# Kernel tuning notes

Measured on AMD Instinct MI355X. Metric: run time of the kernel, lower is better.

## Reference

```python
import jax, jax.numpy as jnp
import numpy as np

DIM = 1024
N_HEADS = 16
HEAD_DIM = DIM // N_HEADS
SCALE = HEAD_DIM ** (-0.5)


def setup_inputs() -> dict:
    key = jax.random.key(0)
    ks = jax.random.split(key, 5)
    B, N = 2, 1024
    x = jax.random.normal(ks[0], (B, N, DIM), dtype=jnp.float32)
    # torch nn.Linear convention: weight is (out_features, in_features)
    w_qkvg = jax.random.normal(ks[1], (4 * DIM, DIM), dtype=jnp.float32) * (DIM ** -0.5)
    b_qkvg = jax.random.normal(ks[2], (4 * DIM,), dtype=jnp.float32) * 0.02
    w_proj = jax.random.normal(ks[3], (DIM, DIM), dtype=jnp.float32) * (DIM ** -0.5)
    b_proj = jax.random.normal(ks[4], (DIM,), dtype=jnp.float32) * 0.02
    return {"x": x, "w_qkvg": w_qkvg, "b_qkvg": b_qkvg, "w_proj": w_proj, "b_proj": b_proj}


def reference(x, w_qkvg, b_qkvg, w_proj, b_proj):
    B, N, dim = x.shape
    # fused qkvg projection: (B, N, 4*dim)
    qkvg = x @ w_qkvg.T + b_qkvg
    # (B, N, 4, H, hd) -> (4, B, H, N, hd)
    qkvg = qkvg.reshape(B, N, 4, N_HEADS, HEAD_DIM).transpose(2, 0, 3, 1, 4)
    q = jax.nn.softplus(qkvg[0])          # (B, H, N, hd)
    k = jax.nn.softplus(qkvg[1])          # (B, H, N, hd)
    v = jax.nn.gelu(qkvg[2], approximate=False)  # (B, H, N, hd)
    g = jax.nn.gelu(qkvg[3], approximate=False)  # (B, H, N, hd)
    # kv = k @ v^T over head_dim -> (B, H, N, N)
    kv = jnp.einsum('bhnd,bhmd->bhnm', k, v)
    # z: contract q over tokens with per-token k-sums -> (B, H, hd)
    z = jnp.einsum('bhcn,bhc->bhn', q, k.sum(axis=-1)) * SCALE
    z = 1.0 / (z + dim)
    # out[b,h,d,n] = sum_c q[b,h,c,n] * kv[b,h,c,d] -> (B, H, N, hd)
    out = jnp.einsum('bhcn,bhcd->bhdn', q, kv) * SCALE
    out = (out + v) * z[:, :, None, :]    # broadcast z over token axis
    out = out.reshape(B, N, dim)          # raw reshape, faithful to original
    out = out * g.reshape(B, N, dim)
    out = out @ w_proj.T + b_proj
    return out
```

## Files before the change

### kernel.cpp

```cpp
#include <hip/hip_runtime.h>
#include <hip/hip_bf16.h>
#include <math.h>

typedef float f32x4 __attribute__((ext_vector_type(4)));
typedef __bf16 bf16_t;
typedef bf16_t bf16x8 __attribute__((ext_vector_type(8)));
typedef bf16_t bf16x4 __attribute__((ext_vector_type(4)));

__device__ __forceinline__ void gload_lds16(const bf16_t* g, bf16_t* l) {
    __builtin_amdgcn_global_load_lds(
        (const __attribute__((address_space(1))) unsigned int*)g,
        (__attribute__((address_space(3))) unsigned int*)l, 16, 0, 0);
}

template<int N_IMM>
__device__ __forceinline__ void wait_vmcnt() {
    if constexpr (N_IMM == 0) asm volatile("s_waitcnt vmcnt(0)" ::: "memory");
    else if constexpr (N_IMM == 2) asm volatile("s_waitcnt vmcnt(2)" ::: "memory");
    else if constexpr (N_IMM == 3) asm volatile("s_waitcnt vmcnt(3)" ::: "memory");
    else if constexpr (N_IMM == 4) asm volatile("s_waitcnt vmcnt(4)" ::: "memory");
    else static_assert(N_IMM == 0, "unsupported vmcnt");
}

__global__ __launch_bounds__(256) void cvt3(const float* __restrict__ a, bf16_t* __restrict__ ao, int na4,
                                            const float* __restrict__ b, bf16_t* __restrict__ bo, int nb4,
                                            const float* __restrict__ c, bf16_t* __restrict__ co, int nc4) {
    int q = blockIdx.x * 256 + threadIdx.x;
    const float* src; bf16_t* dst;
    if (q < na4)            { src = a + (size_t)q * 4;              dst = ao + (size_t)q * 4; }
    else if (q < na4 + nb4) { int r = q - na4; src = b + (size_t)r * 4; dst = bo + (size_t)r * 4; }
    else if (q < na4 + nb4 + nc4) { int r = q - na4 - nb4; src = c + (size_t)r * 4; dst = co + (size_t)r * 4; }
    else return;
    float4 v = *reinterpret_cast<const float4*>(src);
    bf16x4 o;
    o[0] = (bf16_t)v.x; o[1] = (bf16_t)v.y; o[2] = (bf16_t)v.z; o[3] = (bf16_t)v.w;
    *reinterpret_cast<bf16x4*>(dst) = o;
}

template<int BM, int BN, int MR, int NR, int EPI>
__global__ __launch_bounds__(256) void gemm_bt(const bf16_t* __restrict__ A,
                                               const bf16_t* __restrict__ B,
                                               const float* __restrict__ bias,
                                               void* __restrict__ Cout,
                                               int M, int N) {
    constexpr int K = 1024;
    constexpr int TNUM = K / 32;
    constexpr int WCOLS = BN / (NR * 16);
    constexpr int WROWS = BM / (MR * 16);
    static_assert(WROWS * WCOLS == 4, "4 waves");
    constexpr int ASEG = BM / 64, BSEG = BN / 64;
    constexpr int LOADS = ASEG + BSEG;

    __shared__ __align__(16) bf16_t Sa0[BM * 32];
    __shared__ __align__(16) bf16_t Sb0[BN * 32];
    __shared__ __align__(16) bf16_t Sa1[BM * 32];
    __shared__ __align__(16) bf16_t Sb1[BN * 32];
    __shared__ __align__(16) bf16_t Sa2[BM * 32];
    __shared__ __align__(16) bf16_t Sb2[BN * 32];

    const int tid = threadIdx.x;
    const int lane = tid & 63;
    const int w = tid >> 6;
    const int wr = w / WCOLS, wc = w % WCOLS;

    const int NTM = M / BM, NTN = N / BN;
    const int CHM = NTM >> 3;
    const int chunkN = (NTN * CHM) >> 3;
    const int c = blockIdx.x & 7;
    const int pp = blockIdx.x >> 3;
    const int mt = (c % CHM) * 8 + (pp & 7);
    const int nt = (c / CHM) * chunkN + (pp >> 3);
    const int m0 = mt * BM, n0 = nt * BN;

    const int l15 = lane & 15, lg = lane >> 4;
    const int srow = lane >> 2, pos = lane & 3;

    f32x4 acc[MR][NR] = {};

    auto stageTo = [&](bf16_t* Ad, bf16_t* Bd, int k0) {
#pragma unroll
        for (int t = 0; t < ASEG; ++t) {
            int s = w + t * 4;
            int row = s * 16 + srow;
            int ch = pos ^ ((row >> 1) & 3);
            gload_lds16(&A[(size_t)(m0 + row) * K + k0 + ch * 8], &Ad[s * 512]);
        }
#pragma unroll
        for (int t = 0; t < BSEG; ++t) {
            int s = w + t * 4;
            int row = s * 16 + srow;
            int ch = pos ^ ((row >> 1) & 3);
            gload_lds16(&B[(size_t)(n0 + row) * K + k0 + ch * 8], &Bd[s * 512]);
        }
    };

    auto compute = [&](const bf16_t* Ac, const bf16_t* Bc) {
        bf16x8 af[MR], bfr[NR];
#pragma unroll
        for (int i = 0; i < MR; ++i) {
            int ar = wr * MR * 16 + i * 16 + l15;
            af[i] = *(const bf16x8*)(&Ac[ar * 32 + (lg ^ ((ar >> 1) & 3)) * 8]);
        }
#pragma unroll
        for (int j = 0; j < NR; ++j) {
            int br = wc * NR * 16 + j * 16 + l15;
            bfr[j] = *(const bf16x8*)(&Bc[br * 32 + (lg ^ ((br >> 1) & 3)) * 8]);
        }
#pragma unroll
        for (int i = 0; i < MR; ++i)
#pragma unroll
            for (int j = 0; j < NR; ++j)
                acc[i][j] = __builtin_amdgcn_mfma_f32_16x16x32_bf16(af[i], bfr[j], acc[i][j], 0, 0, 0);
    };

    stageTo(Sa0, Sb0, 0);
    stageTo(Sa1, Sb1, 32);

    for (int t = 0; t < TNUM - 2; t += 3) {
        wait_vmcnt<LOADS>();
        __builtin_amdgcn_s_barrier();
        __builtin_amdgcn_sched_barrier(0);
        stageTo(Sa2, Sb2, (t + 2) * 32);
        compute(Sa0, Sb0);
        __builtin_amdgcn_sched_barrier(0);

        wait_vmcnt<LOADS>();
        __builtin_amdgcn_s_barrier();
        __builtin_amdgcn_sched_barrier(0);
        stageTo(Sa0, Sb0, (t + 3) * 32);
        compute(Sa1, Sb1);
        __builtin_amdgcn_sched_barrier(0);

        wait_vmcnt<LOADS>();
        __builtin_amdgcn_s_barrier();
        __builtin_amdgcn_sched_barrier(0);
        stageTo(Sa1, Sb1, (t + 4) * 32);
        compute(Sa2, Sb2);
        __builtin_amdgcn_sched_barrier(0);
    }
    wait_vmcnt<LOADS>();
    __builtin_amdgcn_s_barrier();
    __builtin_amdgcn_sched_barrier(0);
    compute(Sa0, Sb0);
    __builtin_amdgcn_sched_barrier(0);

    wait_vmcnt<0>();
    __builtin_amdgcn_s_barrier();
    __builtin_amdgcn_sched_barrier(0);
    compute(Sa1, Sb1);

#pragma unroll
    for (int i = 0; i < MR; ++i) {
        int gm_base = m0 + wr * MR * 16 + i * 16 + lg * 4;
#pragma unroll
        for (int j = 0; j < NR; ++j) {
            int gn = n0 + wc * NR * 16 + j * 16 + l15;
            float bv = bias[gn];
#pragma unroll
            for (int r = 0; r < 4; ++r) {
                int gm = gm_base + r;
                float v = acc[i][j][r] + bv;
                if (EPI == 0) {
                    float a;
                    if ((gn >> 10) < 2) {
                        a = fmaxf(v, 0.f) + log1pf(expf(-fabsf(v)));
                    } else {
                        a = 0.5f * v * (1.f + erff(v * 0.70710678118654752f));
                    }
                    ((bf16_t*)Cout)[(size_t)gm * N + gn] = (bf16_t)a;
                } else {
                    ((float*)Cout)[(size_t)gm * N + gn] = v;
                }
            }
        }
    }
}

__global__ __launch_bounds__(256) void attn_A(const bf16_t* __restrict__ qkvg,
                                              float* __restrict__ Apart) {
    const int bh = blockIdx.x;
    const int p = blockIdx.y;
    const int b = bh >> 4, h = bh & 15;
    const int tid = threadIdx.x;
    __shared__ float ks[32][64];
    __shared__ float qs[32][64];
    float acc[4][4] = {};
    const int dg = tid >> 4, eg = tid & 15;
    const int stok = tid >> 3, se0 = (tid & 7) * 8;
    const size_t base = ((size_t)b * 1024) * 4096 + (size_t)h * 64;

    for (int t0 = p * 128; t0 < p * 128 + 128; t0 += 32) {
        __syncthreads();
        size_t rowb = base + (size_t)(t0 + stok) * 4096;
        bf16x8 qv8 = *(const bf16x8*)(&qkvg[rowb + se0]);
        bf16x8 kv8 = *(const bf16x8*)(&qkvg[rowb + 1024 + se0]);
#pragma unroll
        for (int jj = 0; jj < 8; ++jj) {
            qs[stok][se0 + jj] = (float)qv8[jj];
            ks[stok][se0 + jj] = (float)kv8[jj];
        }
        __syncthreads();
#pragma unroll 8
        for (int tt = 0; tt < 32; ++tt) {
            f32x4 kv = *(const f32x4*)(&ks[tt][dg * 4]);
            f32x4 qv = *(const f32x4*)(&qs[tt][eg * 4]);
#pragma unroll
            for (int i = 0; i < 4; ++i)
#pragma unroll
                for (int j = 0; j < 4; ++j) acc[i][j] += kv[i] * qv[j];
        }
    }
    float* dst = Apart + ((size_t)p * 32 + bh) * 4096;
#pragma unroll
    for (int i = 0; i < 4; ++i)
#pragma unroll
        for (int j = 0; j < 4; ++j)
            dst[(dg * 4 + i) * 64 + eg * 4 + j] = acc[i][j];
}

__global__ __launch_bounds__(256) void reduce_A_z(const float* __restrict__ Apart,
                                                  float* __restrict__ A,
                                                  float* __restrict__ z) {
    const int bh = blockIdx.x;
    const int tid = threadIdx.x;
    __shared__ float As[4096];
    for (int i0 = tid * 4; i0 < 4096; i0 += 1024) {
        f32x4 s = {};
#pragma unroll
        for (int p = 0; p < 8; ++p) {
            f32x4 v = *(const f32x4*)(&Apart[((size_t)p * 32 + bh) * 4096 + i0]);
            s += v;
        }
        *(f32x4*)(&As[i0]) = s;
        *(f32x4*)(&A[(size_t)bh * 4096 + i0]) = s;
    }
    __syncthreads();
    if (tid < 64) {
        float s = 0.f;
#pragma unroll 8
        for (int d = 0; d < 64; ++d) s += As[d * 64 + tid];
        z[bh * 64 + tid] = 1.0f / (s * 0.125f + 1024.0f);
    }
}

__global__ __launch_bounds__(256) void out_Y(const bf16_t* __restrict__ qkvg,
                                             const float* __restrict__ A,
                                             const float* __restrict__ z,
                                             bf16_t* __restrict__ Y) {
    const int bh = blockIdx.x;
    const int b = bh >> 4, h = bh & 15;
    const int chunk = blockIdx.y;
    const int tid = threadIdx.x;
    __shared__ float As[64][64];
    __shared__ float vs[32][64];
    __shared__ float zs[64];
    for (int i = tid; i < 4096; i += 256) As[i >> 6][i & 63] = A[(size_t)bh * 4096 + i];
    if (tid < 64) zs[tid] = z[bh * 64 + tid];
    const size_t base = ((size_t)b * 1024) * 4096 + (size_t)h * 64;
    const int e = tid & 63, trow = tid >> 6;
    const int stok = tid >> 3, se0 = (tid & 7) * 8;

    for (int t0 = chunk * 64; t0 < chunk * 64 + 64; t0 += 32) {
        __syncthreads();
        bf16x8 vv8 = *(const bf16x8*)(&qkvg[base + (size_t)(t0 + stok) * 4096 + 2048 + se0]);
#pragma unroll
        for (int jj = 0; jj < 8; ++jj) vs[stok][se0 + jj] = (float)vv8[jj];
        __syncthreads();
#pragma unroll
        for (int kk = 0; kk < 8; ++kk) {
            int ml = trow * 8 + kk;
            int m = t0 + ml;
            float s = 0.f;
#pragma unroll 8
            for (int d = 0; d < 64; ++d) s += vs[ml][d] * As[d][e];
            float g = (float)qkvg[base + (size_t)m * 4096 + 3072 + e];
            float o = (s * 0.125f + vs[ml][e]) * zs[e] * g;
            Y[((size_t)b * 1024 + h * 64 + (m >> 4)) * 1024 + ((m & 15) << 6) + e] = (bf16_t)o;
        }
    }
}

extern "C" void kernel_launch(void* const* d_in, const int* in_sizes, int n_in,
                              void* d_out, int out_size, void* d_ws, size_t ws_size,
                              hipStream_t stream) {
    const float* x      = (const float*)d_in[0];
    const float* w_qkvg = (const float*)d_in[1];
    const float* b_qkvg = (const float*)d_in[2];
    const float* w_proj = (const float*)d_in[3];
    const float* b_proj = (const float*)d_in[4];

    char* p = (char*)d_ws;
    bf16_t* xb    = (bf16_t*)p; p += (size_t)2048 * 1024 * 2;
    bf16_t* w1b   = (bf16_t*)p; p += (size_t)4096 * 1024 * 2;
    bf16_t* w2b   = (bf16_t*)p; p += (size_t)1024 * 1024 * 2;
    bf16_t* qkvg  = (bf16_t*)p; p += (size_t)2048 * 4096 * 2;
    float*  Apart = (float*)p;  p += (size_t)8 * 32 * 4096 * 4;
    float*  Afull = (float*)p;  p += (size_t)32 * 4096 * 4;
    float*  zbuf  = (float*)p;  p += (size_t)32 * 64 * 4;
    bf16_t* Ybuf  = (bf16_t*)p; p += (size_t)2048 * 1024 * 2;

    cvt3<<<7168, 256, 0, stream>>>(x, xb, 524288, w_qkvg, w1b, 1048576, w_proj, w2b, 262144);

    gemm_bt<128, 64, 4, 2, 0><<<1024, 256, 0, stream>>>(xb, w1b, b_qkvg, (void*)qkvg, 2048, 4096);
    attn_A<<<dim3(32, 8), 256, 0, stream>>>(qkvg, Apart);
    reduce_A_z<<<32, 256, 0, stream>>>(Apart, Afull, zbuf);
    out_Y<<<dim3(32, 16), 256, 0, stream>>>(qkvg, Afull, zbuf, Ybuf);
    gemm_bt<64, 64, 2, 2, 1><<<512, 256, 0, stream>>>(Ybuf, w2b, b_proj, d_out, 2048, 1024);
}
```

Before: 106.3 us.

## Move activations from QKVG GEMM epilogue into attention kernels with fp32 planar buffer

The fused QKVG projection is split into four separate GEMM launches, each writing a planar fp32 slab for q, k, v and g. Softplus and GELU are no longer applied in the GEMM epilogue; they are computed when the attention kernels load the data. This removes the divergent transcendental epilogue from the GEMM. In exchange, the intermediate buffer doubles in size, the GEMM uses smaller tiles and more launches, and activations are computed inside the attention kernels.

After: 114.4 us. 1.08x slower.

```diff
diff --git a/kernel.cpp b/kernel.cpp
--- a/kernel.cpp
+++ b/kernel.cpp
@@ -6,6 +6,13 @@
 typedef __bf16 bf16_t;
 typedef bf16_t bf16x8 __attribute__((ext_vector_type(8)));
 typedef bf16_t bf16x4 __attribute__((ext_vector_type(4)));
+
+__device__ __forceinline__ float act_softplus(float x) {
+    return fmaxf(x, 0.f) + log1pf(expf(-fabsf(x)));
+}
+__device__ __forceinline__ float act_gelu(float x) {
+    return 0.5f * x * (1.f + erff(x * 0.70710678118654752f));
+}
 
 __device__ __forceinline__ void gload_lds16(const bf16_t* g, bf16_t* l) {
     __builtin_amdgcn_global_load_lds(
@@ -37,11 +44,11 @@
     *reinterpret_cast<bf16x4*>(dst) = o;
 }
 
-template<int BM, int BN, int MR, int NR, int EPI>
+template<int BM, int BN, int MR, int NR>
 __global__ __launch_bounds__(256) void gemm_bt(const bf16_t* __restrict__ A,
                                                const bf16_t* __restrict__ B,
                                                const float* __restrict__ bias,
-                                               void* __restrict__ Cout,
+                                               float* __restrict__ Cout,
                                                int M, int N) {
     constexpr int K = 1024;
     constexpr int TNUM = K / 32;
@@ -159,24 +166,13 @@
 #pragma unroll
             for (int r = 0; r < 4; ++r) {
                 int gm = gm_base + r;
-                float v = acc[i][j][r] + bv;
-                if (EPI == 0) {
-                    float a;
-                    if ((gn >> 10) < 2) {
-                        a = fmaxf(v, 0.f) + log1pf(expf(-fabsf(v)));
-                    } else {
-                        a = 0.5f * v * (1.f + erff(v * 0.70710678118654752f));
-                    }
-                    ((bf16_t*)Cout)[(size_t)gm * N + gn] = (bf16_t)a;
-                } else {
-                    ((float*)Cout)[(size_t)gm * N + gn] = v;
-                }
+                Cout[(size_t)gm * N + gn] = acc[i][j][r] + bv;
             }
         }
     }
 }
 
-__global__ __launch_bounds__(256) void attn_A(const bf16_t* __restrict__ qkvg,
+__global__ __launch_bounds__(256) void attn_A(const float* __restrict__ qkvgf,
                                               float* __restrict__ Apart) {
     const int bh = blockIdx.x;
     const int p = blockIdx.y;
@@ -187,18 +183,24 @@
     float acc[4][4] = {};
     const int dg = tid >> 4, eg = tid & 15;
     const int stok = tid >> 3, se0 = (tid & 7) * 8;
-    const size_t base = ((size_t)b * 1024) * 4096 + (size_t)h * 64;
+    const float* qf = qkvgf;
+    const float* kf = qkvgf + (size_t)2048 * 1024;
 
     for (int t0 = p * 128; t0 < p * 128 + 128; t0 += 32) {
         __syncthreads();
-        size_t rowb = base + (size_t)(t0 + stok) * 4096;
-        bf16x8 qv8 = *(const bf16x8*)(&qkvg[rowb + se0]);
-        bf16x8 kv8 = *(const bf16x8*)(&qkvg[rowb + 1024 + se0]);
-#pragma unroll
-        for (int jj = 0; jj < 8; ++jj) {
-            qs[stok][se0 + jj] = (float)qv8[jj];
-            ks[stok][se0 + jj] = (float)kv8[jj];
-        }
+        size_t rowb = (size_t)(b * 1024 + t0 + stok) * 1024 + h * 64 + se0;
+        float4 q0 = *(const float4*)(&qf[rowb]);
+        float4 q1 = *(const float4*)(&qf[rowb + 4]);
+        float4 k0 = *(const float4*)(&kf[rowb]);
+        float4 k1 = *(const float4*)(&kf[rowb + 4]);
+        qs[stok][se0 + 0] = act_softplus(q0.x); qs[stok][se0 + 1] = act_softplus(q0.y);
+        qs[stok][se0 + 2] = act_softplus(q0.z); qs[stok][se0 + 3] = act_softplus(q0.w);
+        qs[stok][se0 + 4] = act_softplus(q1.x); qs[stok][se0 + 5] = act_softplus(q1.y);
+        qs[stok][se0 + 6] = act_softplus(q1.z); qs[stok][se0 + 7] = act_softplus(q1.w);
+        ks[stok][se0 + 0] = act_softplus(k0.x); ks[stok][se0 + 1] = act_softplus(k0.y);
+        ks[stok][se0 + 2] = act_softplus(k0.z); ks[stok][se0 + 3] = act_softplus(k0.w);
+        ks[stok][se0 + 4] = act_softplus(k1.x); ks[stok][se0 + 5] = act_softplus(k1.y);
+        ks[stok][se0 + 6] = act_softplus(k1.z); ks[stok][se0 + 7] = act_softplus(k1.w);
         __syncthreads();
 #pragma unroll 8
         for (int tt = 0; tt < 32; ++tt) {
@@ -243,7 +245,7 @@
     }
 }
 
-__global__ __launch_bounds__(256) void out_Y(const bf16_t* __restrict__ qkvg,
+__global__ __launch_bounds__(256) void out_Y(const float* __restrict__ qkvgf,
                                              const float* __restrict__ A,
                                              const float* __restrict__ z,
                                              bf16_t* __restrict__ Y) {
@@ -256,15 +258,20 @@
     __shared__ float zs[64];
     for (int i = tid; i < 4096; i += 256) As[i >> 6][i & 63] = A[(size_t)bh * 4096 + i];
     if (tid < 64) zs[tid] = z[bh * 64 + tid];
-    const size_t base = ((size_t)b * 1024) * 4096 + (size_t)h * 64;
+    const float* vf = qkvgf + (size_t)2 * 2048 * 1024;
+    const float* gf = qkvgf + (size_t)3 * 2048 * 1024;
     const int e = tid & 63, trow = tid >> 6;
     const int stok = tid >> 3, se0 = (tid & 7) * 8;
 
     for (int t0 = chunk * 64; t0 < chunk * 64 + 64; t0 += 32) {
         __syncthreads();
-        bf16x8 vv8 = *(const bf16x8*)(&qkvg[base + (size_t)(t0 + stok) * 4096 + 2048 + se0]);
-#pragma unroll
-        for (int jj = 0; jj < 8; ++jj) vs[stok][se0 + jj] = (float)vv8[jj];
+        size_t rowb = (size_t)(b * 1024 + t0 + stok) * 1024 + h * 64 + se0;
+        float4 v0 = *(const float4*)(&vf[rowb]);
+        float4 v1 = *(const float4*)(&vf[rowb + 4]);
+        vs[stok][se0 + 0] = act_gelu(v0.x); vs[stok][se0 + 1] = act_gelu(v0.y);
+        vs[stok][se0 + 2] = act_gelu(v0.z); vs[stok][se0 + 3] = act_gelu(v0.w);
+        vs[stok][se0 + 4] = act_gelu(v1.x); vs[stok][se0 + 5] = act_gelu(v1.y);
+        vs[stok][se0 + 6] = act_gelu(v1.z); vs[stok][se0 + 7] = act_gelu(v1.w);
         __syncthreads();
 #pragma unroll
         for (int kk = 0; kk < 8; ++kk) {
@@ -273,7 +280,7 @@
             float s = 0.f;
 #pragma unroll 8
             for (int d = 0; d < 64; ++d) s += vs[ml][d] * As[d][e];
-            float g = (float)qkvg[base + (size_t)m * 4096 + 3072 + e];
+            float g = act_gelu(gf[(size_t)(b * 1024 + m) * 1024 + h * 64 + e]);
             float o = (s * 0.125f + vs[ml][e]) * zs[e] * g;
             Y[((size_t)b * 1024 + h * 64 + (m >> 4)) * 1024 + ((m & 15) << 6) + e] = (bf16_t)o;
         }
@@ -293,7 +300,7 @@
     bf16_t* xb    = (bf16_t*)p; p += (size_t)2048 * 1024 * 2;
     bf16_t* w1b   = (bf16_t*)p; p += (size_t)4096 * 1024 * 2;
     bf16_t* w2b   = (bf16_t*)p; p += (size_t)1024 * 1024 * 2;
-    bf16_t* qkvg  = (bf16_t*)p; p += (size_t)2048 * 4096 * 2;
+    float*  qkvgf = (float*)p;  p += (size_t)4 * 2048 * 1024 * 4;
     float*  Apart = (float*)p;  p += (size_t)8 * 32 * 4096 * 4;
     float*  Afull = (float*)p;  p += (size_t)32 * 4096 * 4;
     float*  zbuf  = (float*)p;  p += (size_t)32 * 64 * 4;
@@ -301,9 +308,14 @@
 
     cvt3<<<7168, 256, 0, stream>>>(x, xb, 524288, w_qkvg, w1b, 1048576, w_proj, w2b, 262144);
 
-    gemm_bt<128, 64, 4, 2, 0><<<1024, 256, 0, stream>>>(xb, w1b, b_qkvg, (void*)qkvg, 2048, 4096);
-    attn_A<<<dim3(32, 8), 256, 0, stream>>>(qkvg, Apart);
+    for (int s = 0; s < 4; ++s) {
+        gemm_bt<64, 64, 2, 2><<<512, 256, 0, stream>>>(
+            xb, w1b + (size_t)s * 1024 * 1024, b_qkvg + s * 1024,
+            qkvgf + (size_t)s * 2048 * 1024, 2048, 1024);
+    }
+
+    attn_A<<<dim3(32, 8), 256, 0, stream>>>(qkvgf, Apart);
     reduce_A_z<<<32, 256, 0, stream>>>(Apart, Afull, zbuf);
-    out_Y<<<dim3(32, 16), 256, 0, stream>>>(qkvg, Afull, zbuf, Ybuf);
-    gemm_bt<64, 64, 2, 2, 1><<<512, 256, 0, stream>>>(Ybuf, w2b, b_proj, d_out, 2048, 1024);
-}
+    out_Y<<<dim3(32, 16), 256, 0, stream>>>(qkvgf, Afull, zbuf, Ybuf);
+    gemm_bt<64, 64, 2, 2><<<512, 256, 0, stream>>>(Ybuf, w2b, b_proj, (float*)d_out, 2048, 1024);
+}
```

## Split QKVG projection into per-section planar outputs with LDS-staged vector stores

Applied to the files above, without the earlier changes.

Replaces the single 128x64-tile QKVG GEMM with a dedicated 64x64-tile kernel launched over four 1024-wide sections. Each section writes its own contiguous [2048,1024] plane, and the activation is chosen per block by section rather than per element. The epilogue stages activated bf16 values in LDS and writes 16-byte vector stores instead of scattered 2-byte stores. Downstream attention kernels read q/k/v/g from the planar layout with shorter row strides. The smaller tiles give more blocks but less reuse of each A/B tile per block.

After: 94.54 us. 1.12x faster.

```diff
diff --git a/kernel.cpp b/kernel.cpp
--- a/kernel.cpp
+++ b/kernel.cpp
@@ -7,6 +7,13 @@
 typedef bf16_t bf16x8 __attribute__((ext_vector_type(8)));
 typedef bf16_t bf16x4 __attribute__((ext_vector_type(4)));
 
+__device__ __forceinline__ float act_softplus(float x) {
+    return fmaxf(x, 0.f) + log1pf(expf(-fabsf(x)));
+}
+__device__ __forceinline__ float act_gelu(float x) {
+    return 0.5f * x * (1.f + erff(x * 0.70710678118654752f));
+}
+
 __device__ __forceinline__ void gload_lds16(const bf16_t* g, bf16_t* l) {
     __builtin_amdgcn_global_load_lds(
         (const __attribute__((address_space(1))) unsigned int*)g,
@@ -17,7 +24,6 @@
 __device__ __forceinline__ void wait_vmcnt() {
     if constexpr (N_IMM == 0) asm volatile("s_waitcnt vmcnt(0)" ::: "memory");
     else if constexpr (N_IMM == 2) asm volatile("s_waitcnt vmcnt(2)" ::: "memory");
-    else if constexpr (N_IMM == 3) asm volatile("s_waitcnt vmcnt(3)" ::: "memory");
     else if constexpr (N_IMM == 4) asm volatile("s_waitcnt vmcnt(4)" ::: "memory");
     else static_assert(N_IMM == 0, "unsupported vmcnt");
 }
@@ -37,11 +43,142 @@
     *reinterpret_cast<bf16x4*>(dst) = o;
 }
 
-template<int BM, int BN, int MR, int NR, int EPI>
+__global__ __launch_bounds__(256) void gemm_qkvg(const bf16_t* __restrict__ A,
+                                                 const bf16_t* __restrict__ Wall,
+                                                 const float* __restrict__ biasAll,
+                                                 bf16_t* __restrict__ OutAll) {
+    constexpr int BM = 64, BN = 64, MR = 2, NR = 2;
+    constexpr int K = 1024, M = 2048, N = 1024;
+    constexpr int TNUM = K / 32;
+    constexpr int ASEG = 1, BSEG = 1, LOADS = 2;
+
+    __shared__ __align__(16) bf16_t Sa0[BM * 32];
+    __shared__ __align__(16) bf16_t Sb0[BN * 32];
+    __shared__ __align__(16) bf16_t Sa1[BM * 32];
+    __shared__ __align__(16) bf16_t Sb1[BN * 32];
+    __shared__ __align__(16) bf16_t Sa2[BM * 32];
+    __shared__ __align__(16) bf16_t Sb2[BN * 32];
+
+    const int sec = blockIdx.x >> 9;
+    const int bid = blockIdx.x & 511;
+    const bf16_t* B = Wall + (size_t)sec * 1024 * 1024;
+    const float* bias = biasAll + sec * 1024;
+    bf16_t* Cout = OutAll + (size_t)sec * 2048 * 1024;
+
+    const int tid = threadIdx.x;
+    const int lane = tid & 63;
+    const int w = tid >> 6;
+    const int wr = w >> 1, wc = w & 1;
+
+    const int NTM = M / BM, NTN = N / BN;
+    const int CHM = NTM >> 3;
+    const int chunkN = (NTN * CHM) >> 3;
+    const int c = bid & 7;
+    const int pp = bid >> 3;
+    const int mt = (c % CHM) * 8 + (pp & 7);
+    const int nt = (c / CHM) * chunkN + (pp >> 3);
+    const int m0 = mt * BM, n0 = nt * BN;
+
+    const int l15 = lane & 15, lg = lane >> 4;
+    const int srow = lane >> 2, pos = lane & 3;
+
+    f32x4 acc[MR][NR] = {};
+
+    auto stageTo = [&](bf16_t* Ad, bf16_t* Bd, int k0) {
+        {
+            int row = srow;
+            int ch = pos ^ ((row >> 1) & 3);
+            gload_lds16(&A[(size_t)(m0 + w * 16 + row) * K + k0 + ch * 8], &Ad[w * 512]);
+            gload_lds16(&B[(size_t)(n0 + w * 16 + row) * K + k0 + ch * 8], &Bd[w * 512]);
+        }
+    };
+    auto stageTo2 = [&](bf16_t* Ad, bf16_t* Bd, int k0) {
+        int row = w * 16 + srow;
+        int ch = pos ^ ((row >> 1) & 3);
+        gload_lds16(&A[(size_t)(m0 + row) * K + k0 + ch * 8], &Ad[w * 512]);
+        gload_lds16(&B[(size_t)(n0 + row) * K + k0 + ch * 8], &Bd[w * 512]);
+    };
+
+    auto compute = [&](const bf16_t* Ac, const bf16_t* Bc) {
+        bf16x8 af[MR], bfr[NR];
+#pragma unroll
+        for (int i = 0; i < MR; ++i) {
+            int ar = wr * MR * 16 + i * 16 + l15;
+            af[i] = *(const bf16x8*)(&Ac[ar * 32 + (lg ^ ((ar >> 1) & 3)) * 8]);
+        }
+#pragma unroll
+        for (int j = 0; j < NR; ++j) {
+            int br = wc * NR * 16 + j * 16 + l15;
+            bfr[j] = *(const bf16x8*)(&Bc[br * 32 + (lg ^ ((br >> 1) & 3)) * 8]);
+        }
+#pragma unroll
+        for (int i = 0; i < MR; ++i)
+#pragma unroll
+            for (int j = 0; j < NR; ++j)
+                acc[i][j] = __builtin_amdgcn_mfma_f32_16x16x32_bf16(af[i], bfr[j], acc[i][j], 0, 0, 0);
+    };
+
+    stageTo2(Sa0, Sb0, 0);
+    stageTo2(Sa1, Sb1, 32);
+
+    for (int t = 0; t < TNUM - 2; t += 3) {
+        wait_vmcnt<LOADS>();
+        __builtin_amdgcn_s_barrier();
+        __builtin_amdgcn_sched_barrier(0);
+        stageTo2(Sa2, Sb2, (t + 2) * 32);
+        compute(Sa0, Sb0);
+        __builtin_amdgcn_sched_barrier(0);
+
+        wait_vmcnt<LOADS>();
+        __builtin_amdgcn_s_barrier();
+        __builtin_amdgcn_sched_barrier(0);
+        stageTo2(Sa0, Sb0, (t + 3) * 32);
+        compute(Sa1, Sb1);
+        __builtin_amdgcn_sched_barrier(0);
+
+        wait_vmcnt<LOADS>();
+        __builtin_amdgcn_s_barrier();
+        __builtin_amdgcn_sched_barrier(0);
+        stageTo2(Sa1, Sb1, (t + 4) * 32);
+        compute(Sa2, Sb2);
+        __builtin_amdgcn_sched_barrier(0);
+    }
+    wait_vmcnt<LOADS>();
+    __builtin_amdgcn_s_barrier();
+    __builtin_amdgcn_sched_barrier(0);
+    compute(Sa0, Sb0);
+    __builtin_amdgcn_sched_barrier(0);
+
+    wait_vmcnt<0>();
+    __builtin_amdgcn_s_barrier();
+    __builtin_amdgcn_sched_barrier(0);
+    compute(Sa1, Sb1);
+
+    bf16_t* slab = &Sb2[w * 512];
+#pragma unroll
+    for (int i = 0; i < MR; ++i) {
+#pragma unroll
+        for (int j = 0; j < NR; ++j) {
+            int gn = n0 + wc * 32 + j * 16 + l15;
+            float bv = bias[gn];
+#pragma unroll
+            for (int r = 0; r < 4; ++r) {
+                float v = acc[i][j][r] + bv;
+                float a = (sec < 2) ? act_softplus(v) : act_gelu(v);
+                slab[(lg * 4 + r) * 32 + j * 16 + l15] = (bf16_t)a;
+            }
+        }
+        int row = lane >> 2, c8 = (lane & 3) * 8;
+        bf16x8 val = *(const bf16x8*)(&slab[row * 32 + c8]);
+        *(bf16x8*)(&Cout[(size_t)(m0 + wr * 32 + i * 16 + row) * N + n0 + wc * 32 + c8]) = val;
+    }
+}
+
+template<int BM, int BN, int MR, int NR>
 __global__ __launch_bounds__(256) void gemm_bt(const bf16_t* __restrict__ A,
                                                const bf16_t* __restrict__ B,
                                                const float* __restrict__ bias,
-                                               void* __restrict__ Cout,
+                                               float* __restrict__ Cout,
                                                int M, int N) {
     constexpr int K = 1024;
     constexpr int TNUM = K / 32;
@@ -159,24 +296,13 @@
 #pragma unroll
             for (int r = 0; r < 4; ++r) {
                 int gm = gm_base + r;
-                float v = acc[i][j][r] + bv;
-                if (EPI == 0) {
-                    float a;
-                    if ((gn >> 10) < 2) {
-                        a = fmaxf(v, 0.f) + log1pf(expf(-fabsf(v)));
-                    } else {
-                        a = 0.5f * v * (1.f + erff(v * 0.70710678118654752f));
-                    }
-                    ((bf16_t*)Cout)[(size_t)gm * N + gn] = (bf16_t)a;
-                } else {
-                    ((float*)Cout)[(size_t)gm * N + gn] = v;
-                }
+                Cout[(size_t)gm * N + gn] = acc[i][j][r] + bv;
             }
         }
     }
 }
 
-__global__ __launch_bounds__(256) void attn_A(const bf16_t* __restrict__ qkvg,
+__global__ __launch_bounds__(256) void attn_A(const bf16_t* __restrict__ qkvga,
                                               float* __restrict__ Apart) {
     const int bh = blockIdx.x;
     const int p = blockIdx.y;
@@ -187,13 +313,14 @@
     float acc[4][4] = {};
     const int dg = tid >> 4, eg = tid & 15;
     const int stok = tid >> 3, se0 = (tid & 7) * 8;
-    const size_t base = ((size_t)b * 1024) * 4096 + (size_t)h * 64;
+    const bf16_t* qf = qkvga;
+    const bf16_t* kf = qkvga + (size_t)2048 * 1024;
 
     for (int t0 = p * 128; t0 < p * 128 + 128; t0 += 32) {
         __syncthreads();
-        size_t rowb = base + (size_t)(t0 + stok) * 4096;
-        bf16x8 qv8 = *(const bf16x8*)(&qkvg[rowb + se0]);
-        bf16x8 kv8 = *(const bf16x8*)(&qkvg[rowb + 1024 + se0]);
+        size_t rowb = (size_t)(b * 1024 + t0 + stok) * 1024 + h * 64 + se0;
+        bf16x8 qv8 = *(const bf16x8*)(&qf[rowb]);
+        bf16x8 kv8 = *(const bf16x8*)(&kf[rowb]);
 #pragma unroll
         for (int jj = 0; jj < 8; ++jj) {
             qs[stok][se0 + jj] = (float)qv8[jj];
@@ -243,7 +370,7 @@
     }
 }
 
-__global__ __launch_bounds__(256) void out_Y(const bf16_t* __restrict__ qkvg,
+__global__ __launch_bounds__(256) void out_Y(const bf16_t* __restrict__ qkvga,
                                              const float* __restrict__ A,
                                              const float* __restrict__ z,
                                              bf16_t* __restrict__ Y) {
@@ -256,13 +383,14 @@
     __shared__ float zs[64];
     for (int i = tid; i < 4096; i += 256) As[i >> 6][i & 63] = A[(size_t)bh * 4096 + i];
     if (tid < 64) zs[tid] = z[bh * 64 + tid];
-    const size_t base = ((size_t)b * 1024) * 4096 + (size_t)h * 64;
+    const bf16_t* vf = qkvga + (size_t)2 * 2048 * 1024;
+    const bf16_t* gf = qkvga + (size_t)3 * 2048 * 1024;
     const int e = tid & 63, trow = tid >> 6;
     const int stok = tid >> 3, se0 = (tid & 7) * 8;
 
     for (int t0 = chunk * 64; t0 < chunk * 64 + 64; t0 += 32) {
         __syncthreads();
-        bf16x8 vv8 = *(const bf16x8*)(&qkvg[base + (size_t)(t0 + stok) * 4096 + 2048 + se0]);
+        bf16x8 vv8 = *(const bf16x8*)(&vf[(size_t)(b * 1024 + t0 + stok) * 1024 + h * 64 + se0]);
 #pragma unroll
         for (int jj = 0; jj < 8; ++jj) vs[stok][se0 + jj] = (float)vv8[jj];
         __syncthreads();
@@ -273,7 +401,7 @@
             float s = 0.f;
 #pragma unroll 8
             for (int d = 0; d < 64; ++d) s += vs[ml][d] * As[d][e];
-            float g = (float)qkvg[base + (size_t)m * 4096 + 3072 + e];
+            float g = (float)gf[(size_t)(b * 1024 + m) * 1024 + h * 64 + e];
             float o = (s * 0.125f + vs[ml][e]) * zs[e] * g;
             Y[((size_t)b * 1024 + h * 64 + (m >> 4)) * 1024 + ((m & 15) << 6) + e] = (bf16_t)o;
         }
@@ -293,7 +421,7 @@
     bf16_t* xb    = (bf16_t*)p; p += (size_t)2048 * 1024 * 2;
     bf16_t* w1b   = (bf16_t*)p; p += (size_t)4096 * 1024 * 2;
     bf16_t* w2b   = (bf16_t*)p; p += (size_t)1024 * 1024 * 2;
-    bf16_t* qkvg  = (bf16_t*)p; p += (size_t)2048 * 4096 * 2;
+    bf16_t* qkvga = (bf16_t*)p; p += (size_t)4 * 2048 * 1024 * 2;
     float*  Apart = (float*)p;  p += (size_t)8 * 32 * 4096 * 4;
     float*  Afull = (float*)p;  p += (size_t)32 * 4096 * 4;
     float*  zbuf  = (float*)p;  p += (size_t)32 * 64 * 4;
@@ -301,9 +429,10 @@
 
     cvt3<<<7168, 256, 0, stream>>>(x, xb, 524288, w_qkvg, w1b, 1048576, w_proj, w2b, 262144);
 
-    gemm_bt<128, 64, 4, 2, 0><<<1024, 256, 0, stream>>>(xb, w1b, b_qkvg, (void*)qkvg, 2048, 4096);
-    attn_A<<<dim3(32, 8), 256, 0, stream>>>(qkvg, Apart);
+    gemm_qkvg<<<2048, 256, 0, stream>>>(xb, w1b, b_qkvg, qkvga);
+
+    attn_A<<<dim3(32, 8), 256, 0, stream>>>(qkvga, Apart);
     reduce_A_z<<<32, 256, 0, stream>>>(Apart, Afull, zbuf);
-    out_Y<<<dim3(32, 16), 256, 0, stream>>>(qkvg, Afull, zbuf, Ybuf);
-    gemm_bt<64, 64, 2, 2, 1><<<512, 256, 0, stream>>>(Ybuf, w2b, b_proj, d_out, 2048, 1024);
-}
+    out_Y<<<dim3(32, 16), 256, 0, stream>>>(qkvga, Afull, zbuf, Ybuf);
+    gemm_bt<64, 64, 2, 2><<<512, 256, 0, stream>>>(Ybuf, w2b, b_proj, (float*)d_out, 2048, 1024);
+}
```
